# Kernel tuning notes

Measured on AMD Instinct MI355X. Metric: run time of the kernel, lower is better.

The kernel has to match this reference:

```python
import jax, jax.numpy as jnp
import numpy as np
import math

MODEL_DIM = 1024
DIM_K = 128
DIM_V = 128
BATCH = 8
SEQ = 2048


def setup_inputs() -> dict:
    key = jax.random.key(0)
    ks = jax.random.split(key, 6)
    return {
        "query": jax.random.normal(ks[0], (BATCH, SEQ, MODEL_DIM), dtype=jnp.float32),
        "key": jax.random.normal(ks[1], (BATCH, SEQ, MODEL_DIM), dtype=jnp.float32),
        "value": jax.random.normal(ks[2], (BATCH, SEQ, MODEL_DIM), dtype=jnp.float32),
        "Wq": jax.random.normal(ks[3], (MODEL_DIM, DIM_K), dtype=jnp.float32) * (1.0 / math.sqrt(MODEL_DIM)),
        "Wk": jax.random.normal(ks[4], (MODEL_DIM, DIM_K), dtype=jnp.float32) * (1.0 / math.sqrt(MODEL_DIM)),
        "Wv": jax.random.normal(ks[5], (MODEL_DIM, DIM_V), dtype=jnp.float32) * (1.0 / math.sqrt(MODEL_DIM)),
    }


def reference(query, key, value, Wq, Wk, Wv):
    # Projections (nn.Linear with bias=False): x @ W, W stored as [in, out]
    q = jnp.einsum("bsm,mk->bsk", query, Wq)   # [B, S, dim_k]
    k = jnp.einsum("bsm,mk->bsk", key, Wk)     # [B, S, dim_k]
    v = jnp.einsum("bsm,mv->bsv", value, Wv)   # [B, S, dim_v]

    scale = 1.0 / math.sqrt(DIM_K)
    scores = jnp.einsum("bqk,bsk->bqs", q, k) * scale  # [B, S, S]

    # is_causal=True: mask strictly-upper triangle with -inf
    seq = scores.shape[-1]
    causal = jnp.tril(jnp.ones((seq, seq), dtype=bool))  # True = keep
    scores = jnp.where(causal[None, :, :], scores, -jnp.inf)

    attn = jax.nn.softmax(scores, axis=-1)
    # NaN-fix: rows with all -inf produce NaN -> set to 0 (faithful to masked_fill of NaNs)
    attn = jnp.where(jnp.isnan(attn), 0.0, attn)

    out = jnp.einsum("bqs,bsv->bqv", attn, v)  # [B, S, dim_v]
    return out
```

## Files before the change

kernel.cpp:

```cpp
#include <hip/hip_runtime.h>
#include <hip/hip_bf16.h>
#include <math.h>

typedef short bf16x8 __attribute__((ext_vector_type(8)));
typedef float f32x4 __attribute__((ext_vector_type(4)));
typedef unsigned int u32x4 __attribute__((ext_vector_type(4)));
typedef unsigned int u32x2 __attribute__((ext_vector_type(2)));

#define SEQ 2048
#define MD 1024
#define DH 128

__device__ __forceinline__ unsigned f2b(float f) {
  union { __hip_bfloat16 h; unsigned short u; } c;
  c.h = __float2bfloat16(f);
  return (unsigned)c.u;
}

__global__ __launch_bounds__(256) void wprep_kernel(
    const float* __restrict__ wq, const float* __restrict__ wk,
    const float* __restrict__ wv, __hip_bfloat16* __restrict__ wt)
{
  const int proj = blockIdx.x;
  const int part = blockIdx.y;
  const float* __restrict__ w = (proj == 0) ? wq : ((proj == 1) ? wk : wv);
  __hip_bfloat16* __restrict__ o = wt + (size_t)proj * (128 * 1024);
  __shared__ __hip_bfloat16 t[128 * 130];
  const int tid = threadIdx.x;
#pragma unroll 4
  for (int i = 0; i < 64; ++i) {
    int idx = i * 256 + tid;
    int kl = idx >> 7, n = idx & 127;
    t[kl * 130 + n] = __float2bfloat16(w[(size_t)(part * 128 + kl) * 128 + n]);
  }
  __syncthreads();
#pragma unroll 4
  for (int j = 0; j < 64; ++j) {
    int idx = j * 256 + tid;
    int n = idx >> 7, kl = idx & 127;
    o[(size_t)n * 1024 + part * 128 + kl] = t[kl * 130 + n];
  }
}

__global__ __launch_bounds__(256) void proj_kernel(
    const float* __restrict__ xq, const float* __restrict__ xk, const float* __restrict__ xv,
    const __hip_bfloat16* __restrict__ wt,
    __hip_bfloat16* __restrict__ q_ws, __hip_bfloat16* __restrict__ k_ws,
    __hip_bfloat16* __restrict__ vt_ws)
{
  const int proj = blockIdx.y;
  const float* __restrict__ x = (proj == 0) ? xq : ((proj == 1) ? xk : xv);
  const __hip_bfloat16* __restrict__ w = wt + (size_t)proj * (128 * 1024);
  const int m0 = blockIdx.x * 64;
  const int tid = threadIdx.x;
  const int lane = tid & 63;
  const int wid = tid >> 6;
  const int ll = lane & 15, lh = lane >> 4;
  const int wr = (wid >> 1) * 32;
  const int wc = (wid & 1) * 64;

  __shared__ char lds[2][24 * 1024];

  const f32x4 zero4 = {0.f, 0.f, 0.f, 0.f};
  f32x4 acc[2][4];
#pragma unroll
  for (int mi = 0; mi < 2; ++mi)
#pragma unroll
    for (int nf = 0; nf < 4; ++nf) acc[mi][nf] = zero4;

  const int a_row = tid >> 4;
  const int a_c4  = (tid & 15) << 2;
  const int b_n   = tid >> 3;
  const int b_c   = (tid & 7) << 3;

  f32x4 ar[4];
  u32x4 br[4];

#define LD_TILES(KT)                                                          \
  {                                                                           \
    _Pragma("unroll")                                                         \
    for (int i = 0; i < 4; ++i)                                               \
      ar[i] = *reinterpret_cast<const f32x4*>(                                \
          &x[(size_t)(m0 + a_row + i * 16) * MD + (KT) * 64 + a_c4]);         \
    _Pragma("unroll")                                                         \
    for (int j = 0; j < 4; ++j)                                               \
      br[j] = *reinterpret_cast<const u32x4*>(                                \
          &w[(size_t)(b_n + j * 32) * MD + (KT) * 64 + b_c]);                 \
  }

#define ST_TILES(BUF)                                                         \
  {                                                                           \
    char* Asb = lds[BUF];                                                     \
    char* Bsb = lds[BUF] + 8192;                                              \
    _Pragma("unroll")                                                         \
    for (int i = 0; i < 4; ++i) {                                             \
      int row = a_row + i * 16;                                               \
      u32x2 pk;                                                               \
      pk[0] = f2b(ar[i][0]) | (f2b(ar[i][1]) << 16);                          \
      pk[1] = f2b(ar[i][2]) | (f2b(ar[i][3]) << 16);                          \
      *reinterpret_cast<u32x2*>(Asb + row * 128 +                             \
          ((a_c4 << 1) ^ ((row & 7) << 4))) = pk;                             \
    }                                                                         \
    _Pragma("unroll")                                                         \
    for (int j = 0; j < 4; ++j) {                                             \
      int n = b_n + j * 32;                                                   \
      *reinterpret_cast<u32x4*>(Bsb + n * 128 +                               \
          ((b_c << 1) ^ ((n & 7) << 4))) = br[j];                             \
    }                                                                         \
  }

  LD_TILES(0);
  ST_TILES(0);
  __syncthreads();

  for (int kt = 0; kt < 16; ++kt) {
    const int cur = kt & 1;
    if (kt < 15) LD_TILES(kt + 1);
    {
      char* Asb = lds[cur];
      char* Bsb = lds[cur] + 8192;
#pragma unroll
      for (int kk = 0; kk < 2; ++kk) {
        bf16x8 af[2], bfv[4];
#pragma unroll
        for (int mi = 0; mi < 2; ++mi) {
          int row = wr + mi * 16 + ll;
          af[mi] = *reinterpret_cast<bf16x8*>(
              Asb + row * 128 + ((kk * 64 + lh * 16) ^ ((row & 7) << 4)));
        }
#pragma unroll
        for (int nf = 0; nf < 4; ++nf) {
          int n = wc + nf * 16 + ll;
          bfv[nf] = *reinterpret_cast<bf16x8*>(
              Bsb + n * 128 + ((kk * 64 + lh * 16) ^ ((n & 7) << 4)));
        }
#pragma unroll
        for (int mi = 0; mi < 2; ++mi)
#pragma unroll
          for (int nf = 0; nf < 4; ++nf)
            acc[mi][nf] = __builtin_amdgcn_mfma_f32_16x16x32_bf16(
                af[mi], bfv[nf], acc[mi][nf], 0, 0, 0);
      }
    }
    if (kt < 15) ST_TILES(1 - cur);
    __syncthreads();
  }
#undef LD_TILES
#undef ST_TILES

  if (proj < 2) {
    __hip_bfloat16* __restrict__ outp = proj ? k_ws : q_ws;
#pragma unroll
    for (int mi = 0; mi < 2; ++mi)
#pragma unroll
      for (int nf = 0; nf < 4; ++nf) {
        int col = wc + nf * 16 + ll;
#pragma unroll
        for (int r = 0; r < 4; ++r) {
          int row = m0 + wr + mi * 16 + lh * 4 + r;
          union { __hip_bfloat16 h; unsigned short u; } c;
          c.u = (unsigned short)f2b(acc[mi][nf][r]);
          outp[(size_t)row * DH + col] = c.h;
        }
      }
  } else {
    const int b = m0 >> 11, sb = m0 & 2047;
#pragma unroll
    for (int mi = 0; mi < 2; ++mi)
#pragma unroll
      for (int nf = 0; nf < 4; ++nf) {
        int s = sb + wr + mi * 16 + lh * 4;
        int d = wc + nf * 16 + ll;
        u32x2 pk;
        pk[0] = f2b(acc[mi][nf][0]) | (f2b(acc[mi][nf][1]) << 16);
        pk[1] = f2b(acc[mi][nf][2]) | (f2b(acc[mi][nf][3]) << 16);
        *reinterpret_cast<u32x2*>(&vt_ws[((size_t)b * DH + d) * SEQ + s]) = pk;
      }
  }
}

__global__ __launch_bounds__(256) void attn_kernel(
    const __hip_bfloat16* __restrict__ q_ws, const __hip_bfloat16* __restrict__ k_ws,
    const __hip_bfloat16* __restrict__ vt_ws,
    float* __restrict__ pO, float* __restrict__ pml)
{
  const int s = blockIdx.x;
  int qt, c;
  if (s < 8)       { qt = s;                c = 0; }
  else if (s < 24) { int u = s - 8;  qt = 8 + (u >> 1);  c = u & 1; }
  else if (s < 48) { int u = s - 24; qt = 16 + u / 3;    c = u % 3; }
  else             { int u = s - 48; qt = 24 + (u >> 2); c = u & 3; }
  const int b = blockIdx.y;
  const int g = qt >> 3;
  const int slot = b * 80 + (4 * g * (g + 1) + (g + 1) * (qt & 7)) + c;

  const int tid = threadIdx.x;
  const int lane = tid & 63;
  const int wid = tid >> 6;
  const int ll = lane & 15;
  const int lh = lane >> 4;

  __shared__ __hip_bfloat16 Ks[64 * 128];
  __shared__ __hip_bfloat16 Vs[128 * 64];
  __shared__ float Ps[64 * 64];
  char* Ksb = (char*)Ks;
  char* Vsb = (char*)Vs;
  char* Psb = (char*)Ps;

  bf16x8 qf[4];
  {
    const size_t qbase = ((size_t)b * SEQ + qt * 64 + wid * 16 + ll) * DH;
#pragma unroll
    for (int kk = 0; kk < 4; ++kk)
      qf[kk] = *reinterpret_cast<const bf16x8*>(&q_ws[qbase + kk * 32 + lh * 8]);
  }

  const f32x4 zero4 = {0.f, 0.f, 0.f, 0.f};
  float m_r[4], l_r[4];
  f32x4 oacc[8];
#pragma unroll
  for (int r = 0; r < 4; ++r) { m_r[r] = -INFINITY; l_r[r] = 0.f; }
#pragma unroll
  for (int nd = 0; nd < 8; ++nd) oacc[nd] = zero4;

  const float sl2e = 0.0883883476483184f * 1.4426950408889634f;

  const int it0 = c * 8;
  const int it1 = min(qt + 1, it0 + 8);
  for (int it = it0; it < it1; ++it) {
    const int kv0 = it * 64;
#pragma unroll
    for (int i = 0; i < 4; ++i) {
      int id = tid + i * 256;
      int row = id >> 4;
      int cb = (id & 15) << 4;
      u32x4 v = *reinterpret_cast<const u32x4*>(
          &k_ws[((size_t)b * SEQ + kv0 + row) * DH + (cb >> 1)]);
      *reinterpret_cast<u32x4*>(Ksb + row * 256 + (cb ^ ((row & 7) << 4))) = v;
    }
#pragma unroll
    for (int i = 0; i < 4; ++i) {
      int id = tid + i * 256;
      int d = id >> 3;
      int cb = (id & 7) << 4;
      u32x4 v = *reinterpret_cast<const u32x4*>(
          &vt_ws[((size_t)b * DH + d) * SEQ + kv0 + (cb >> 1)]);
      *reinterpret_cast<u32x4*>(Vsb + d * 128 + (cb ^ ((d & 7) << 4))) = v;
    }
    __syncthreads();

    f32x4 sacc[4];
#pragma unroll
    for (int nf = 0; nf < 4; ++nf) sacc[nf] = zero4;
#pragma unroll
    for (int nf = 0; nf < 4; ++nf) {
      int row = nf * 16 + ll;
#pragma unroll
      for (int kk = 0; kk < 4; ++kk) {
        bf16x8 kf = *reinterpret_cast<bf16x8*>(
            Ksb + row * 256 + ((kk * 64 + lh * 16) ^ ((row & 7) << 4)));
        sacc[nf] = __builtin_amdgcn_mfma_f32_16x16x32_bf16(qf[kk], kf, sacc[nf], 0, 0, 0);
      }
    }

    float sv[4][4];
    const int qr0 = qt * 64 + wid * 16 + lh * 4;
#pragma unroll
    for (int nf = 0; nf < 4; ++nf) {
      int kc = kv0 + nf * 16 + ll;
#pragma unroll
      for (int r = 0; r < 4; ++r) {
        float sc = sacc[nf][r] * sl2e;
        sv[nf][r] = (kc <= qr0 + r) ? sc : -INFINITY;
      }
    }

    float p[4][4];
    float alpha[4];
#pragma unroll
    for (int r = 0; r < 4; ++r) {
      float mx = fmaxf(fmaxf(sv[0][r], sv[1][r]), fmaxf(sv[2][r], sv[3][r]));
#pragma unroll
      for (int off = 1; off < 16; off <<= 1)
        mx = fmaxf(mx, __shfl_xor(mx, off));
      float mnew = fmaxf(m_r[r], mx);
      float sum = 0.f;
#pragma unroll
      for (int nf = 0; nf < 4; ++nf) {
        float pv = exp2f(sv[nf][r] - mnew);
        p[nf][r] = pv;
        sum += pv;
      }
#pragma unroll
      for (int off = 1; off < 16; off <<= 1)
        sum += __shfl_xor(sum, off);
      alpha[r] = exp2f(m_r[r] - mnew);
      l_r[r] = l_r[r] * alpha[r] + sum;
      m_r[r] = mnew;
    }
#pragma unroll
    for (int nd = 0; nd < 8; ++nd)
#pragma unroll
      for (int r = 0; r < 4; ++r) oacc[nd][r] *= alpha[r];

#pragma unroll
    for (int nf = 0; nf < 4; ++nf) {
      int kv = nf * 16 + ll;
      f32x4 pv4 = {p[nf][0], p[nf][1], p[nf][2], p[nf][3]};
      *reinterpret_cast<f32x4*>(
          Psb + kv * 256 + ((wid * 64 + lh * 16) ^ ((kv & 7) << 4))) = pv4;
    }

#pragma unroll
    for (int kf = 0; kf < 2; ++kf) {
      float pf[8];
#pragma unroll
      for (int j = 0; j < 8; ++j) {
        int kv = kf * 32 + lh * 8 + j;
        pf[j] = *reinterpret_cast<float*>(
            Psb + kv * 256 + ((wid * 64 + ll * 4) ^ ((kv & 7) << 4)));
      }
      bf16x8 pa;
#pragma unroll
      for (int j = 0; j < 8; ++j) pa[j] = (short)f2b(pf[j]);
#pragma unroll
      for (int nd = 0; nd < 8; ++nd) {
        int d = nd * 16 + ll;
        bf16x8 vf = *reinterpret_cast<bf16x8*>(
            Vsb + d * 128 + ((kf * 64 + lh * 16) ^ ((d & 7) << 4)));
        oacc[nd] = __builtin_amdgcn_mfma_f32_16x16x32_bf16(pa, vf, oacc[nd], 0, 0, 0);
      }
    }
    __syncthreads();
  }

  float* __restrict__ po = pO + (size_t)slot * (64 * 128);
#pragma unroll
  for (int nd = 0; nd < 8; ++nd) {
    int d = nd * 16 + ll;
#pragma unroll
    for (int r = 0; r < 4; ++r) {
      int row = wid * 16 + lh * 4 + r;
      po[row * 128 + d] = oacc[nd][r];
    }
  }
  if (ll == 0) {
    float* __restrict__ pm = pml + (size_t)slot * 128;
#pragma unroll
    for (int r = 0; r < 4; ++r) {
      int row = wid * 16 + lh * 4 + r;
      pm[row * 2 + 0] = m_r[r];
      pm[row * 2 + 1] = l_r[r];
    }
  }
}

__global__ __launch_bounds__(256) void combine_kernel(
    const float* __restrict__ pO, const float* __restrict__ pml,
    float* __restrict__ out)
{
  const int qt = blockIdx.x;
  const int b = blockIdx.y;
  const int g = qt >> 3;
  const int nc = g + 1;
  const size_t slot0 = (size_t)b * 80 + (4 * g * (g + 1) + (g + 1) * (qt & 7));
  const int tid = threadIdx.x;
  const int r = tid >> 2;
  const int q4 = tid & 3;

  float m[4], l[4];
#pragma unroll
  for (int i = 0; i < 4; ++i) {
    if (i < nc) {
      m[i] = pml[(slot0 + i) * 128 + r * 2 + 0];
      l[i] = pml[(slot0 + i) * 128 + r * 2 + 1];
    } else { m[i] = -INFINITY; l[i] = 0.f; }
  }
  float M = fmaxf(fmaxf(m[0], m[1]), fmaxf(m[2], m[3]));
  float w[4];
  float L = 0.f;
#pragma unroll
  for (int i = 0; i < 4; ++i) {
    w[i] = (i < nc) ? exp2f(m[i] - M) : 0.f;
    L += l[i] * w[i];
  }
  const float inv = 1.0f / L;

  const size_t orow = ((size_t)b * SEQ + qt * 64 + r) * DH;
#pragma unroll
  for (int j = 0; j < 8; ++j) {
    const int col = q4 * 32 + j * 4;
    f32x4 acc = {0.f, 0.f, 0.f, 0.f};
#pragma unroll
    for (int i = 0; i < 4; ++i) {
      if (i < nc) {
        f32x4 v = *reinterpret_cast<const f32x4*>(
            &pO[(slot0 + i) * (64 * 128) + r * 128 + col]);
#pragma unroll
        for (int u = 0; u < 4; ++u) acc[u] += v[u] * w[i];
      }
    }
#pragma unroll
    for (int u = 0; u < 4; ++u) acc[u] *= inv;
    *reinterpret_cast<f32x4*>(&out[orow + col]) = acc;
  }
}

extern "C" void kernel_launch(void* const* d_in, const int* in_sizes, int n_in,
                              void* d_out, int out_size, void* d_ws, size_t ws_size,
                              hipStream_t stream) {
  const float* xq = (const float*)d_in[0];
  const float* xk = (const float*)d_in[1];
  const float* xv = (const float*)d_in[2];
  const float* wq = (const float*)d_in[3];
  const float* wk = (const float*)d_in[4];
  const float* wv = (const float*)d_in[5];

  __hip_bfloat16* q_ws = (__hip_bfloat16*)d_ws;
  __hip_bfloat16* k_ws = q_ws + (size_t)16384 * 128;
  __hip_bfloat16* vt_ws = k_ws + (size_t)16384 * 128;
  __hip_bfloat16* wt_ws = vt_ws + (size_t)16384 * 128;
  float* pO = (float*)((char*)d_ws + 13369344);
  float* pml = (float*)((char*)d_ws + 13369344 + 20971520);
  float* out = (float*)d_out;

  wprep_kernel<<<dim3(3, 8), 256, 0, stream>>>(wq, wk, wv, wt_ws);
  proj_kernel<<<dim3(256, 3), 256, 0, stream>>>(xq, xk, xv, wt_ws,
                                                q_ws, k_ws, vt_ws);
  attn_kernel<<<dim3(80, 8), 256, 0, stream>>>(q_ws, k_ws, vt_ws, pO, pml);
  combine_kernel<<<dim3(32, 8), 256, 0, stream>>>(pO, pml, out);
}
```

Before: 103.1 us.

## Restructure projection GEMM with direct global-to-LDS loads and smaller M tiles

The projection kernel now uses 32-row M tiles (double the block count) and stages the fp32 activation tile straight into a swizzled LDS buffer with global_load_lds, converting to bf16 only when building MFMA fragments. Weight fragments are read directly from global memory (via cache) instead of being staged in LDS. This removes the register round trip and LDS staging of the B tile and aims to raise occupancy and parallelism for this memory-bound projection. In exchange, double buffering is dropped: each k-step waits on vmcnt(0) and a barrier before computing, so load latency is exposed, and weight data is re-read from L2 by every block.

```diff
diff --git a/kernel.cpp b/kernel.cpp
--- a/kernel.cpp
+++ b/kernel.cpp
@@ -15,6 +15,12 @@
   union { __hip_bfloat16 h; unsigned short u; } c;
   c.h = __float2bfloat16(f);
   return (unsigned)c.u;
+}
+
+__device__ __forceinline__ void cp16(void* lds_base, const void* gsrc) {
+  __builtin_amdgcn_global_load_lds(
+      (const __attribute__((address_space(1))) unsigned int*)gsrc,
+      (__attribute__((address_space(3))) unsigned int*)lds_base, 16, 0, 0);
 }
 
 __global__ __launch_bounds__(256) void wprep_kernel(
@@ -51,131 +57,93 @@
   const int proj = blockIdx.y;
   const float* __restrict__ x = (proj == 0) ? xq : ((proj == 1) ? xk : xv);
   const __hip_bfloat16* __restrict__ w = wt + (size_t)proj * (128 * 1024);
-  const int m0 = blockIdx.x * 64;
+  const int m0 = blockIdx.x * 32;
   const int tid = threadIdx.x;
   const int lane = tid & 63;
   const int wid = tid >> 6;
   const int ll = lane & 15, lh = lane >> 4;
-  const int wr = (wid >> 1) * 32;
+  const int wr = (wid >> 1) * 16;
   const int wc = (wid & 1) * 64;
 
-  __shared__ char lds[2][24 * 1024];
+  __shared__ float Af[32 * 64];
+  char* Afb = (char*)Af;
 
   const f32x4 zero4 = {0.f, 0.f, 0.f, 0.f};
-  f32x4 acc[2][4];
-#pragma unroll
-  for (int mi = 0; mi < 2; ++mi)
-#pragma unroll
-    for (int nf = 0; nf < 4; ++nf) acc[mi][nf] = zero4;
-
-  const int a_row = tid >> 4;
-  const int a_c4  = (tid & 15) << 2;
-  const int b_n   = tid >> 3;
-  const int b_c   = (tid & 7) << 3;
-
-  f32x4 ar[4];
-  u32x4 br[4];
-
-#define LD_TILES(KT)                                                          \
-  {                                                                           \
-    _Pragma("unroll")                                                         \
-    for (int i = 0; i < 4; ++i)                                               \
-      ar[i] = *reinterpret_cast<const f32x4*>(                                \
-          &x[(size_t)(m0 + a_row + i * 16) * MD + (KT) * 64 + a_c4]);         \
-    _Pragma("unroll")                                                         \
-    for (int j = 0; j < 4; ++j)                                               \
-      br[j] = *reinterpret_cast<const u32x4*>(                                \
-          &w[(size_t)(b_n + j * 32) * MD + (KT) * 64 + b_c]);                 \
-  }
-
-#define ST_TILES(BUF)                                                         \
-  {                                                                           \
-    char* Asb = lds[BUF];                                                     \
-    char* Bsb = lds[BUF] + 8192;                                              \
-    _Pragma("unroll")                                                         \
-    for (int i = 0; i < 4; ++i) {                                             \
-      int row = a_row + i * 16;                                               \
-      u32x2 pk;                                                               \
-      pk[0] = f2b(ar[i][0]) | (f2b(ar[i][1]) << 16);                          \
-      pk[1] = f2b(ar[i][2]) | (f2b(ar[i][3]) << 16);                          \
-      *reinterpret_cast<u32x2*>(Asb + row * 128 +                             \
-          ((a_c4 << 1) ^ ((row & 7) << 4))) = pk;                             \
-    }                                                                         \
-    _Pragma("unroll")                                                         \
-    for (int j = 0; j < 4; ++j) {                                             \
-      int n = b_n + j * 32;                                                   \
-      *reinterpret_cast<u32x4*>(Bsb + n * 128 +                               \
-          ((b_c << 1) ^ ((n & 7) << 4))) = br[j];                             \
-    }                                                                         \
-  }
-
-  LD_TILES(0);
-  ST_TILES(0);
-  __syncthreads();
+  f32x4 acc[4];
+#pragma unroll
+  for (int nf = 0; nf < 4; ++nf) acc[nf] = zero4;
+
+  int srow[2], scol[2];
+#pragma unroll
+  for (int c = 0; c < 2; ++c) {
+    int o = (wid * 2 + c) * 1024 + lane * 16;
+    int row = o >> 8;
+    int slot = (o >> 4) & 15;
+    srow[c] = row;
+    scol[c] = (slot ^ (row & 15)) << 2;
+  }
+  const int r = wr + ll;
+  const int rsw = (r & 15);
+
+  const __hip_bfloat16* __restrict__ wb[4];
+#pragma unroll
+  for (int nf = 0; nf < 4; ++nf)
+    wb[nf] = w + (size_t)(wc + nf * 16 + ll) * MD + lh * 8;
 
   for (int kt = 0; kt < 16; ++kt) {
-    const int cur = kt & 1;
-    if (kt < 15) LD_TILES(kt + 1);
-    {
-      char* Asb = lds[cur];
-      char* Bsb = lds[cur] + 8192;
-#pragma unroll
-      for (int kk = 0; kk < 2; ++kk) {
-        bf16x8 af[2], bfv[4];
-#pragma unroll
-        for (int mi = 0; mi < 2; ++mi) {
-          int row = wr + mi * 16 + ll;
-          af[mi] = *reinterpret_cast<bf16x8*>(
-              Asb + row * 128 + ((kk * 64 + lh * 16) ^ ((row & 7) << 4)));
-        }
-#pragma unroll
-        for (int nf = 0; nf < 4; ++nf) {
-          int n = wc + nf * 16 + ll;
-          bfv[nf] = *reinterpret_cast<bf16x8*>(
-              Bsb + n * 128 + ((kk * 64 + lh * 16) ^ ((n & 7) << 4)));
-        }
-#pragma unroll
-        for (int mi = 0; mi < 2; ++mi)
-#pragma unroll
-          for (int nf = 0; nf < 4; ++nf)
-            acc[mi][nf] = __builtin_amdgcn_mfma_f32_16x16x32_bf16(
-                af[mi], bfv[nf], acc[mi][nf], 0, 0, 0);
-      }
-    }
-    if (kt < 15) ST_TILES(1 - cur);
+    cp16(Afb + (wid * 2 + 0) * 1024,
+         &x[(size_t)(m0 + srow[0]) * MD + kt * 64 + scol[0]]);
+    cp16(Afb + (wid * 2 + 1) * 1024,
+         &x[(size_t)(m0 + srow[1]) * MD + kt * 64 + scol[1]]);
+    asm volatile("s_waitcnt vmcnt(0)" ::: "memory");
     __syncthreads();
-  }
-#undef LD_TILES
-#undef ST_TILES
+
+#pragma unroll
+    for (int kk = 0; kk < 2; ++kk) {
+      const int s0 = kk * 8 + lh * 2;
+      f32x4 a0 = *reinterpret_cast<f32x4*>(
+          Afb + r * 256 + (((s0    ) ^ rsw) << 4));
+      f32x4 a1 = *reinterpret_cast<f32x4*>(
+          Afb + r * 256 + (((s0 + 1) ^ rsw) << 4));
+      bf16x8 af;
+#pragma unroll
+      for (int j = 0; j < 4; ++j) {
+        af[j]     = (short)f2b(a0[j]);
+        af[4 + j] = (short)f2b(a1[j]);
+      }
+#pragma unroll
+      for (int nf = 0; nf < 4; ++nf) {
+        bf16x8 bv = *reinterpret_cast<const bf16x8*>(wb[nf] + kt * 64 + kk * 32);
+        acc[nf] = __builtin_amdgcn_mfma_f32_16x16x32_bf16(af, bv, acc[nf], 0, 0, 0);
+      }
+    }
+    __syncthreads();
+  }
 
   if (proj < 2) {
     __hip_bfloat16* __restrict__ outp = proj ? k_ws : q_ws;
 #pragma unroll
-    for (int mi = 0; mi < 2; ++mi)
-#pragma unroll
-      for (int nf = 0; nf < 4; ++nf) {
-        int col = wc + nf * 16 + ll;
-#pragma unroll
-        for (int r = 0; r < 4; ++r) {
-          int row = m0 + wr + mi * 16 + lh * 4 + r;
-          union { __hip_bfloat16 h; unsigned short u; } c;
-          c.u = (unsigned short)f2b(acc[mi][nf][r]);
-          outp[(size_t)row * DH + col] = c.h;
-        }
-      }
+    for (int nf = 0; nf < 4; ++nf) {
+      int col = wc + nf * 16 + ll;
+#pragma unroll
+      for (int q = 0; q < 4; ++q) {
+        int row = m0 + wr + lh * 4 + q;
+        union { __hip_bfloat16 h; unsigned short u; } c;
+        c.u = (unsigned short)f2b(acc[nf][q]);
+        outp[(size_t)row * DH + col] = c.h;
+      }
+    }
   } else {
     const int b = m0 >> 11, sb = m0 & 2047;
 #pragma unroll
-    for (int mi = 0; mi < 2; ++mi)
-#pragma unroll
-      for (int nf = 0; nf < 4; ++nf) {
-        int s = sb + wr + mi * 16 + lh * 4;
-        int d = wc + nf * 16 + ll;
-        u32x2 pk;
-        pk[0] = f2b(acc[mi][nf][0]) | (f2b(acc[mi][nf][1]) << 16);
-        pk[1] = f2b(acc[mi][nf][2]) | (f2b(acc[mi][nf][3]) << 16);
-        *reinterpret_cast<u32x2*>(&vt_ws[((size_t)b * DH + d) * SEQ + s]) = pk;
-      }
+    for (int nf = 0; nf < 4; ++nf) {
+      int s = sb + wr + lh * 4;
+      int d = wc + nf * 16 + ll;
+      u32x2 pk;
+      pk[0] = f2b(acc[nf][0]) | (f2b(acc[nf][1]) << 16);
+      pk[1] = f2b(acc[nf][2]) | (f2b(acc[nf][3]) << 16);
+      *reinterpret_cast<u32x2*>(&vt_ws[((size_t)b * DH + d) * SEQ + s]) = pk;
+    }
   }
 }
 
@@ -219,7 +187,7 @@
   float m_r[4], l_r[4];
   f32x4 oacc[8];
 #pragma unroll
-  for (int r = 0; r < 4; ++r) { m_r[r] = -INFINITY; l_r[r] = 0.f; }
+  for (int q = 0; q < 4; ++q) { m_r[q] = -INFINITY; l_r[q] = 0.f; }
 #pragma unroll
   for (int nd = 0; nd < 8; ++nd) oacc[nd] = zero4;
 
@@ -269,39 +237,39 @@
     for (int nf = 0; nf < 4; ++nf) {
       int kc = kv0 + nf * 16 + ll;
 #pragma unroll
-      for (int r = 0; r < 4; ++r) {
-        float sc = sacc[nf][r] * sl2e;
-        sv[nf][r] = (kc <= qr0 + r) ? sc : -INFINITY;
+      for (int q = 0; q < 4; ++q) {
+        float sc = sacc[nf][q] * sl2e;
+        sv[nf][q] = (kc <= qr0 + q) ? sc : -INFINITY;
       }
     }
 
     float p[4][4];
     float alpha[4];
 #pragma unroll
-    for (int r = 0; r < 4; ++r) {
-      float mx = fmaxf(fmaxf(sv[0][r], sv[1][r]), fmaxf(sv[2][r], sv[3][r]));
+    for (int q = 0; q < 4; ++q) {
+      float mx = fmaxf(fmaxf(sv[0][q], sv[1][q]), fmaxf(sv[2][q], sv[3][q]));
 #pragma unroll
       for (int off = 1; off < 16; off <<= 1)
         mx = fmaxf(mx, __shfl_xor(mx, off));
-      float mnew = fmaxf(m_r[r], mx);
+      float mnew = fmaxf(m_r[q], mx);
       float sum = 0.f;
 #pragma unroll
       for (int nf = 0; nf < 4; ++nf) {
-        float pv = exp2f(sv[nf][r] - mnew);
-        p[nf][r] = pv;
+        float pv = exp2f(sv[nf][q] - mnew);
+        p[nf][q] = pv;
         sum += pv;
       }
 #pragma unroll
       for (int off = 1; off < 16; off <<= 1)
         sum += __shfl_xor(sum, off);
-      alpha[r] = exp2f(m_r[r] - mnew);
-      l_r[r] = l_r[r] * alpha[r] + sum;
-      m_r[r] = mnew;
+      alpha[q] = exp2f(m_r[q] - mnew);
+      l_r[q] = l_r[q] * alpha[q] + sum;
+      m_r[q] = mnew;
     }
 #pragma unroll
     for (int nd = 0; nd < 8; ++nd)
 #pragma unroll
-      for (int r = 0; r < 4; ++r) oacc[nd][r] *= alpha[r];
+      for (int q = 0; q < 4; ++q) oacc[nd][q] *= alpha[q];
 
 #pragma unroll
     for (int nf = 0; nf < 4; ++nf) {
@@ -339,18 +307,18 @@
   for (int nd = 0; nd < 8; ++nd) {
     int d = nd * 16 + ll;
 #pragma unroll
-    for (int r = 0; r < 4; ++r) {
-      int row = wid * 16 + lh * 4 + r;
-      po[row * 128 + d] = oacc[nd][r];
+    for (int q = 0; q < 4; ++q) {
+      int row = wid * 16 + lh * 4 + q;
+      po[row * 128 + d] = oacc[nd][q];
     }
   }
   if (ll == 0) {
     float* __restrict__ pm = pml + (size_t)slot * 128;
 #pragma unroll
-    for (int r = 0; r < 4; ++r) {
-      int row = wid * 16 + lh * 4 + r;
-      pm[row * 2 + 0] = m_r[r];
-      pm[row * 2 + 1] = l_r[r];
+    for (int q = 0; q < 4; ++q) {
+      int row = wid * 16 + lh * 4 + q;
+      pm[row * 2 + 0] = m_r[q];
+      pm[row * 2 + 1] = l_r[q];
     }
   }
 }
@@ -425,7 +393,7 @@
   float* out = (float*)d_out;
 
   wprep_kernel<<<dim3(3, 8), 256, 0, stream>>>(wq, wk, wv, wt_ws);
-  proj_kernel<<<dim3(256, 3), 256, 0, stream>>>(xq, xk, xv, wt_ws,
+  proj_kernel<<<dim3(512, 3), 256, 0, stream>>>(xq, xk, xv, wt_ws,
                                                 q_ws, k_ws, vt_ws);
   attn_kernel<<<dim3(80, 8), 256, 0, stream>>>(q_ws, k_ws, vt_ws, pO, pml);
   combine_kernel<<<dim3(32, 8), 256, 0, stream>>>(pO, pml, out);
```

After: 167.4 us. 62.4% more time.
